# Kernel optimization log

Hardware: AMD Instinct MI355X
Metric: run time of the kernel (lower is better)

The kernel has to match this reference:

```python
import jax, jax.numpy as jnp
import numpy as np
from math import ceil

N = 20000   # nodes
E = 320000  # edges
D = 128     # num_features == num_hidden
K = ceil(N * 0.1)  # 2000 PMA seeds


def _gcn(x, W, b, src, dst):
    # PyG GCNConv: add self-loops, symmetric deg^-1/2 normalization, sum-aggregate, bias
    n = x.shape[0]
    sl = jnp.arange(n)
    s = jnp.concatenate([src, sl])
    d = jnp.concatenate([dst, sl])
    deg = jax.ops.segment_sum(jnp.ones((s.shape[0],), x.dtype), d, num_segments=n)
    dinv = jax.lax.rsqrt(jnp.maximum(deg, 1e-12))
    norm = dinv[s] * dinv[d]
    h = x @ W
    return jax.ops.segment_sum(h[s] * norm[:, None], d, num_segments=n) + b


def _ln(x, g, b):
    m = jnp.mean(x, -1, keepdims=True)
    v = jnp.var(x, -1, keepdims=True)
    return (x - m) * jax.lax.rsqrt(v + 1e-5) * g + b


def setup_inputs() -> dict:
    key = jax.random.key(0)
    ks = jax.random.split(key, 32)
    w = lambda i, shape: jax.random.normal(ks[i], shape, jnp.float32) * 0.05
    z = lambda shape: jnp.zeros(shape, jnp.float32)
    o = lambda shape: jnp.ones(shape, jnp.float32)
    return {
        "x": jax.random.normal(ks[0], (N, D), jnp.float32),
        "edge_index": jax.random.randint(ks[1], (2, E), 0, N),
        "batch": jnp.zeros((N,), jnp.int32),
        "W1": w(2, (D, D)), "b1": z((D,)),
        "W2": w(3, (D, D)), "b2": z((D,)),
        "S": w(4, (1, K, D)),
        "Wq": w(5, (D, D)), "bq": z((D,)),
        "Wk": w(6, (D, D)), "bk": z((D,)),
        "Wv": w(7, (D, D)), "bv": z((D,)),
        "Wo": w(8, (D, D)), "bo": z((D,)),
        "g0": o((D,)), "be0": z((D,)),
        "g1": o((D,)), "be1": z((D,)),
        "Wl": w(9, (D, D)), "bl": z((D,)),
        "W3": w(10, (D, D)), "b3": z((D,)),
        "W4": w(11, (D, D)), "b4": z((D,)),
        "W5": w(12, (D, D)), "b5": z((D,)),
    }


def reference(x, edge_index, batch, W1, b1, W2, b2, S, Wq, bq, Wk, bk, Wv, bv,
              Wo, bo, g0, be0, g1, be1, Wl, bl, W3, b3, W4, b4, W5, b5):
    src, dst = edge_index[0], edge_index[1]
    h = jax.nn.relu(_gcn(x, W1, b1, src, dst))
    h = jax.nn.relu(_gcn(h, W2, b2, src, dst))
    # B=1 dense batch: mask all-true -> additive attention mask is 0
    Q = S @ Wq + bq                        # [1,K,D]
    Kd = _gcn(h, Wk, bk, src, dst)[None]   # [1,N,D]  (mab_conv='GCN')
    Vd = _gcn(h, Wv, bv, src, dst)[None]   # [1,N,D]
    score = jnp.einsum('bkd,bnd->bkn', Q, Kd) / jnp.sqrt(jnp.float32(D))
    A = jax.nn.softmax(score, axis=1)      # cluster=True: softmax over seed dim
    out = Q + jnp.einsum('bkn,bnd->bkd', A, Vd)
    out = _ln(out, g0, be0)
    out = out + jax.nn.relu(out @ Wo + bo)
    out = _ln(out, g1, be1)
    xl = out @ Wl + bl                     # [1,K,D]
    x_out = jnp.einsum('bkn,bkd->bnd', A, xl)[0]  # attn^T @ x -> [N,D], mask all-true
    h = jax.nn.relu(_gcn(x_out, W3, b3, src, dst))
    h = jax.nn.relu(_gcn(h, W4, b4, src, dst))
    return _gcn(h, W5, b5, src, dst)       # [N,D]
```

## Files before the change

### kernel.cpp

```cpp
#include <hip/hip_runtime.h>

#define NN 20000
#define EE 320000
#define KK 2000
#define KP 2048
#define SCALE 0.08838834764831845f
#define ZSPLIT 16
#define ACHUNKS 625

typedef const float* cfp;
typedef __attribute__((ext_vector_type(8))) short sh8;
typedef __attribute__((ext_vector_type(4))) float f32x4;

static __device__ __forceinline__ float4 ld4(const float* p){ return *reinterpret_cast<const float4*>(p); }
static __device__ __forceinline__ void st4(float* p, float4 v){ *reinterpret_cast<float4*>(p) = v; }

static __device__ __forceinline__ unsigned short f2bf(float f){
    unsigned int u = __float_as_uint(f);
    u = (u + 0x7FFFu + ((u >> 16) & 1u)) >> 16;
    return (unsigned short)u;
}
static __device__ __forceinline__ float bf2f(unsigned short h){
    return __uint_as_float(((unsigned int)h) << 16);
}
static __device__ __forceinline__ sh8 lds8(const unsigned short* p){ return *reinterpret_cast<const sh8*>(p); }

__global__ __launch_bounds__(256) void k_count(const int* dst, int* deg){
    int i = blockIdx.x*256 + threadIdx.x;
    if (i < EE) atomicAdd(&deg[dst[i]], 1);
}

__global__ __launch_bounds__(256) void k_dinv(const int* deg, float* dinv){
    int n = blockIdx.x*256 + threadIdx.x;
    if (n < NN) dinv[n] = rsqrtf((float)deg[n] + 1.0f);
}

__global__ __launch_bounds__(1024) void k_scan(const int* cnt, int* rows){
    __shared__ int part[1024];
    int t = threadIdx.x;
    int base = t*20;
    int s = 0;
    for (int i = 0; i < 20; ++i){ int idx = base+i; if (idx < NN) s += cnt[idx]; }
    part[t] = s; __syncthreads();
    for (int off = 1; off < 1024; off <<= 1){
        int v = (t >= off) ? part[t-off] : 0;
        __syncthreads();
        part[t] += v;
        __syncthreads();
    }
    int run = part[t] - s;
    for (int i = 0; i < 20; ++i){
        int idx = base+i;
        if (idx < NN){ rows[idx] = run; run += cnt[idx]; }
    }
    if (t == 0) rows[NN] = EE;
}

__global__ __launch_bounds__(256) void k_fill(const int* src, const int* dst, const int* rows,
                                              int* cursor, int* col){
    int i = blockIdx.x*256 + threadIdx.x;
    if (i < EE){
        int d = dst[i];
        int pos = rows[d] + atomicAdd(&cursor[d], 1);
        col[pos] = src[i];
    }
}

__global__ __launch_bounds__(256) void conv_wT(cfp w0, cfp w1, cfp w2, cfp w3, cfp w4, cfp w5, cfp w6,
                                               unsigned short* wts){
    const float* in;
    switch (blockIdx.z){
        case 0: in = w0; break; case 1: in = w1; break; case 2: in = w2; break;
        case 3: in = w3; break; case 4: in = w4; break; case 5: in = w5; break;
        default: in = w6; break;
    }
    unsigned short* out = wts + (size_t)blockIdx.z*16384;
    __shared__ float t[64][65];
    int r0 = blockIdx.x*64, c0 = blockIdx.y*64;
    int tid = threadIdx.x;
    for (int i = tid; i < 64*16; i += 256){
        int r = i >> 4, c4 = (i & 15) * 4;
        float4 v = ld4(in + (size_t)(r0+r)*128 + c0 + c4);
        t[r][c4+0]=v.x; t[r][c4+1]=v.y; t[r][c4+2]=v.z; t[r][c4+3]=v.w;
    }
    __syncthreads();
    for (int i = tid; i < 64*16; i += 256){
        int c = i >> 4, r4 = (i & 15) * 4;
        ushort4 o;
        o.x = f2bf(t[r4+0][c]); o.y = f2bf(t[r4+1][c]);
        o.z = f2bf(t[r4+2][c]); o.w = f2bf(t[r4+3][c]);
        *reinterpret_cast<ushort4*>(out + (size_t)(c0+c)*128 + r0 + r4) = o;
    }
}

__global__ __launch_bounds__(512) void gemm128(const float* __restrict__ A, const float* __restrict__ Wm,
                                               float* __restrict__ C, int M,
                                               const float* bias, const float* resid, int relu){
    __shared__ __align__(16) float Ws[128*132];
    __shared__ float As[64*129];
    int tid = threadIdx.x;
    int r0 = blockIdx.x*64;
    for (int i = tid; i < 128*32; i += 512){
        int r = i >> 5, c4 = (i & 31) * 4;
        float4 v = ld4(Wm + r*128 + c4);
        st4(&Ws[r*132 + c4], v);
    }
    for (int i = tid; i < 64*32; i += 512){
        int r = i >> 5, c4 = (i & 31) * 4;
        float4 v = (r0 + r < M) ? ld4(A + (size_t)(r0+r)*128 + c4) : make_float4(0,0,0,0);
        As[r*129 + c4+0] = v.x; As[r*129 + c4+1] = v.y;
        As[r*129 + c4+2] = v.z; As[r*129 + c4+3] = v.w;
    }
    __syncthreads();
    int a = tid >> 5;
    int b = tid & 31;
    float acc[4][4] = {};
    #pragma unroll 4
    for (int d = 0; d < 128; ++d){
        float4 w = ld4(&Ws[d*132 + 4*b]);
        float wv[4] = {w.x, w.y, w.z, w.w};
        float av[4];
        #pragma unroll
        for (int i = 0; i < 4; ++i) av[i] = As[(4*a+i)*129 + d];
        #pragma unroll
        for (int i = 0; i < 4; ++i)
            #pragma unroll
            for (int j = 0; j < 4; ++j)
                acc[i][j] += av[i]*wv[j];
    }
    int cc = 4*b;
    #pragma unroll
    for (int i = 0; i < 4; ++i){
        int r = r0 + 4*a + i;
        if (r < M){
            float v[4];
            #pragma unroll
            for (int j = 0; j < 4; ++j) v[j] = acc[i][j];
            if (bias){
                #pragma unroll
                for (int j = 0; j < 4; ++j) v[j] += bias[cc+j];
            }
            if (relu){
                #pragma unroll
                for (int j = 0; j < 4; ++j) v[j] = fmaxf(v[j], 0.f);
            }
            if (resid){
                float4 rv = ld4(resid + (size_t)r*128 + cc);
                v[0]+=rv.x; v[1]+=rv.y; v[2]+=rv.z; v[3]+=rv.w;
            }
            st4(C + (size_t)r*128 + cc, make_float4(v[0],v[1],v[2],v[3]));
        }
    }
}

__global__ __launch_bounds__(256) void tgemm(const unsigned short* __restrict__ A, int M,
                                             const unsigned short* __restrict__ Wt,
                                             const float* __restrict__ rscale,
                                             unsigned short* __restrict__ C){
    int tid = threadIdx.x;
    int wave = tid >> 6, lane = tid & 63;
    int wm = wave >> 1, wn = wave & 1;
    int m_base = blockIdx.x*64 + wm*32;
    int n_base = blockIdx.y*64 + wn*32;
    int l15 = lane & 15;
    int roff = (lane >> 4) * 8;
    const unsigned short* ap0 = A + (size_t)(m_base + l15)*128 + roff;
    const unsigned short* ap1 = ap0 + 16*128;
    const unsigned short* b0p = Wt + (size_t)(n_base + l15)*128 + roff;
    const unsigned short* b1p = b0p + 16*128;
    f32x4 acc00 = (f32x4)0.f, acc01 = (f32x4)0.f, acc10 = (f32x4)0.f, acc11 = (f32x4)0.f;
    #pragma unroll
    for (int r = 0; r < 128; r += 32){
        sh8 a0 = lds8(ap0 + r);
        sh8 a1 = lds8(ap1 + r);
        sh8 b0 = lds8(b0p + r);
        sh8 b1 = lds8(b1p + r);
        acc00 = __builtin_amdgcn_mfma_f32_16x16x32_bf16(a0, b0, acc00, 0, 0, 0);
        acc01 = __builtin_amdgcn_mfma_f32_16x16x32_bf16(a0, b1, acc01, 0, 0, 0);
        acc10 = __builtin_amdgcn_mfma_f32_16x16x32_bf16(a1, b0, acc10, 0, 0, 0);
        acc11 = __builtin_amdgcn_mfma_f32_16x16x32_bf16(a1, b1, acc11, 0, 0, 0);
    }
    int rq = (lane >> 4) * 4;
    f32x4 accs[2][2] = {{acc00, acc01},{acc10, acc11}};
    #pragma unroll
    for (int mi = 0; mi < 2; ++mi){
        #pragma unroll
        for (int ni = 0; ni < 2; ++ni){
            f32x4 a = accs[mi][ni];
            int gn = n_base + ni*16 + l15;
            #pragma unroll
            for (int reg = 0; reg < 4; ++reg){
                int gm = m_base + mi*16 + rq + reg;
                if (gm < M) C[(size_t)gm*128 + gn] = f2bf(a[reg] * (rscale ? rscale[gm] : 1.f));
            }
        }
    }
}

__global__ __launch_bounds__(256) void gcn_agg_bf(const unsigned short* __restrict__ y, const float* __restrict__ dinv,
                                                  const int* __restrict__ rows, const int* __restrict__ col,
                                                  const float* __restrict__ bias, void* __restrict__ outv,
                                                  int relu, int out_fp32){
    int wid = (int)((blockIdx.x*256 + threadIdx.x) >> 6);
    int lane = threadIdx.x & 63;
    if (wid >= NN) return;
    int f = lane*2;
    ushort2 u = *reinterpret_cast<const ushort2*>(y + (size_t)wid*128 + f);
    float ax = bf2f(u.x), ay = bf2f(u.y);
    int s = rows[wid], e = rows[wid+1];
    int j = s;
    int e4 = s + ((e - s) & ~3);
    for (; j < e4; j += 4){
        int c0 = col[j], c1 = col[j+1], c2 = col[j+2], c3 = col[j+3];
        ushort2 v0 = *reinterpret_cast<const ushort2*>(y + (size_t)c0*128 + f);
        ushort2 v1 = *reinterpret_cast<const ushort2*>(y + (size_t)c1*128 + f);
        ushort2 v2 = *reinterpret_cast<const ushort2*>(y + (size_t)c2*128 + f);
        ushort2 v3 = *reinterpret_cast<const ushort2*>(y + (size_t)c3*128 + f);
        ax += bf2f(v0.x) + bf2f(v1.x) + bf2f(v2.x) + bf2f(v3.x);
        ay += bf2f(v0.y) + bf2f(v1.y) + bf2f(v2.y) + bf2f(v3.y);
    }
    for (; j < e; ++j){
        int c0 = col[j];
        ushort2 v0 = *reinterpret_cast<const ushort2*>(y + (size_t)c0*128 + f);
        ax += bf2f(v0.x); ay += bf2f(v0.y);
    }
    float dn = dinv[wid];
    float ox = ax*dn + bias[f];
    float oy = ay*dn + bias[f+1];
    if (relu){ ox = fmaxf(ox, 0.f); oy = fmaxf(oy, 0.f); }
    if (out_fp32){
        *reinterpret_cast<float2*>((float*)outv + (size_t)wid*128 + f) = make_float2(ox, oy);
    } else {
        ushort2 o; o.x = f2bf(ox); o.y = f2bf(oy);
        *reinterpret_cast<ushort2*>((unsigned short*)outv + (size_t)wid*128 + f) = o;
    }
}

__global__ __launch_bounds__(256) void conv_bf16(const float* __restrict__ in, unsigned short* __restrict__ out, int n4){
    int i = blockIdx.x*256 + threadIdx.x;
    if (i < n4){
        float4 v = ld4(in + (size_t)i*4);
        ushort4 o;
        o.x = f2bf(v.x); o.y = f2bf(v.y); o.z = f2bf(v.z); o.w = f2bf(v.w);
        *reinterpret_cast<ushort4*>(out + (size_t)i*4) = o;
    }
}

__global__ __launch_bounds__(256) void conv_bf16_T(const float* __restrict__ in, unsigned short* __restrict__ out,
                                                   int M, int ldout, const float* __restrict__ rscale){
    __shared__ float t[64][65];
    int r0 = blockIdx.x*64, c0 = blockIdx.y*64;
    int tid = threadIdx.x;
    for (int i = tid; i < 64*16; i += 256){
        int r = i >> 4, c4 = (i & 15) * 4;
        float4 v = (r0 + r < M) ? ld4(in + (size_t)(r0+r)*128 + c0 + c4) : make_float4(0,0,0,0);
        if (rscale && r0 + r < M){
            float sc = rscale[r0 + r];
            v.x *= sc; v.y *= sc; v.z *= sc; v.w *= sc;
        }
        t[r][c4+0]=v.x; t[r][c4+1]=v.y; t[r][c4+2]=v.z; t[r][c4+3]=v.w;
    }
    __syncthreads();
    for (int i = tid; i < 64*16; i += 256){
        int c = i >> 4, r4 = (i & 15) * 4;
        if (r0 + r4 < M){
            ushort4 o;
            o.x = f2bf(t[r4+0][c]); o.y = f2bf(t[r4+1][c]);
            o.z = f2bf(t[r4+2][c]); o.w = f2bf(t[r4+3][c]);
            *reinterpret_cast<ushort4*>(out + (size_t)(c0+c)*ldout + r0 + r4) = o;
        }
    }
}

__global__ __launch_bounds__(256) void k_rcp32(const float* __restrict__ zp, float* __restrict__ zinv){
    int n = blockIdx.x*256 + threadIdx.x;
    if (n < NN){
        float s = 0.f;
        #pragma unroll
        for (int y = 0; y < 32; ++y) s += zp[(size_t)y*NN + n];
        zinv[n] = 1.f / s;
    }
}

__global__ __launch_bounds__(256) void s_gemm_exp(const unsigned short* __restrict__ Kb,
                                                  const unsigned short* __restrict__ Qb2,
                                                  unsigned short* __restrict__ E, float* __restrict__ zpart){
    __shared__ unsigned short Es[64*68];
    int tid = threadIdx.x;
    int wave = tid >> 6, lane = tid & 63;
    int wm = wave >> 1, wn = wave & 1;
    int n_blk = blockIdx.x*64, k_blk = blockIdx.y*64;
    int l15 = lane & 15;
    int roff = (lane >> 4) * 8;
    const unsigned short* ap0 = Kb + (size_t)(n_blk + wm*32 + l15)*128 + roff;
    const unsigned short* ap1 = ap0 + 16*128;
    const unsigned short* bp0 = Qb2 + (size_t)(k_blk + wn*32 + l15)*128 + roff;
    const unsigned short* bp1 = bp0 + 16*128;
    f32x4 acc00 = (f32x4)0.f, acc01 = (f32x4)0.f, acc10 = (f32x4)0.f, acc11 = (f32x4)0.f;
    #pragma unroll
    for (int r = 0; r < 128; r += 32){
        sh8 a0 = lds8(ap0 + r);
        sh8 a1 = lds8(ap1 + r);
        sh8 b0 = lds8(bp0 + r);
        sh8 b1 = lds8(bp1 + r);
        acc00 = __builtin_amdgcn_mfma_f32_16x16x32_bf16(a0, b0, acc00, 0, 0, 0);
        acc01 = __builtin_amdgcn_mfma_f32_16x16x32_bf16(a0, b1, acc01, 0, 0, 0);
        acc10 = __builtin_amdgcn_mfma_f32_16x16x32_bf16(a1, b0, acc10, 0, 0, 0);
        acc11 = __builtin_amdgcn_mfma_f32_16x16x32_bf16(a1, b1, acc11, 0, 0, 0);
    }
    int rq = (lane >> 4) * 4;
    f32x4 accs[2][2] = {{acc00, acc01},{acc10, acc11}};
    #pragma unroll
    for (int mi = 0; mi < 2; ++mi){
        #pragma unroll
        for (int ni = 0; ni < 2; ++ni){
            f32x4 a = accs[mi][ni];
            int c_loc = wn*32 + ni*16 + l15;
            bool kv = (k_blk + c_loc) < KK;
            #pragma unroll
            for (int reg = 0; reg < 4; ++reg){
                int r_loc = wm*32 + mi*16 + rq + reg;
                float e = kv ? __expf(a[reg]*SCALE) : 0.f;
                Es[r_loc*68 + c_loc] = f2bf(e);
            }
        }
    }
    __syncthreads();
    if (tid < 64){
        int n = n_blk + tid;
        if (n < NN){
            float s = 0.f;
            #pragma unroll 8
            for (int j = 0; j < 64; ++j) s += bf2f(Es[tid*68 + j]);
            zpart[(size_t)blockIdx.y*NN + n] = s;
        }
    }
    for (int i = tid; i < 512; i += 256){
        int r = i >> 3, c8 = (i & 7) * 8;
        if (n_blk + r < NN){
            ushort4 lo = *reinterpret_cast<const ushort4*>(&Es[r*68 + c8]);
            ushort4 hi = *reinterpret_cast<const ushort4*>(&Es[r*68 + c8 + 4]);
            unsigned short* dst = E + (size_t)(n_blk + r)*KP + k_blk + c8;
            *reinterpret_cast<ushort4*>(dst) = lo;
            *reinterpret_cast<ushort4*>(dst + 4) = hi;
        }
    }
}

__global__ __launch_bounds__(256) void attn_gemm(const unsigned short* __restrict__ E,
                                                 const unsigned short* __restrict__ Vt,
                                                 float* __restrict__ part){
    __shared__ unsigned short As[64*36];
    int tid = threadIdx.x;
    int wave = tid >> 6, lane = tid & 63;
    int kk0 = blockIdx.x*64;
    int per = (ACHUNKS + ZSPLIT - 1) / ZSPLIT;
    int c0 = blockIdx.y*per;
    int c1 = min(ACHUNKS, c0 + per);
    int l15 = lane & 15;
    int q8 = (lane >> 4) * 8;
    int d0 = wave*32;
    int n_l = tid & 31;
    int k8 = (tid >> 5) * 8;
    f32x4 acc[4][2];
    #pragma unroll
    for (int g = 0; g < 4; ++g){ acc[g][0] = (f32x4)0.f; acc[g][1] = (f32x4)0.f; }
    const unsigned short* ebase = E + (size_t)n_l*KP + kk0 + k8;
    const unsigned short* vb0p = Vt + (size_t)(d0 + l15)*NN + q8;
    const unsigned short* vb1p = vb0p + (size_t)16*NN;
    sh8 etmp = lds8(ebase + (size_t)c0*32*KP);
    sh8 vb0 = lds8(vb0p + c0*32);
    sh8 vb1 = lds8(vb1p + c0*32);
    for (int ch = c0; ch < c1; ++ch){
        unsigned short tmp[8];
        *reinterpret_cast<sh8*>(tmp) = etmp;
        #pragma unroll
        for (int j = 0; j < 8; ++j) As[(k8 + j)*36 + n_l] = tmp[j];
        __syncthreads();
        sh8 etn = (sh8)0, vbn0 = (sh8)0, vbn1 = (sh8)0;
        if (ch + 1 < c1){
            etn  = lds8(ebase + (size_t)(ch+1)*32*KP);
            vbn0 = lds8(vb0p + (ch+1)*32);
            vbn1 = lds8(vb1p + (ch+1)*32);
        }
        #pragma unroll
        for (int g = 0; g < 4; ++g){
            const unsigned short* ap = &As[(g*16 + l15)*36 + q8];
            union { struct { ushort4 lo, hi; } u; sh8 v; } af;
            af.u.lo = *reinterpret_cast<const ushort4*>(ap);
            af.u.hi = *reinterpret_cast<const ushort4*>(ap + 4);
            acc[g][0] = __builtin_amdgcn_mfma_f32_16x16x32_bf16(af.v, vb0, acc[g][0], 0, 0, 0);
            acc[g][1] = __builtin_amdgcn_mfma_f32_16x16x32_bf16(af.v, vb1, acc[g][1], 0, 0, 0);
        }
        __syncthreads();
        etmp = etn; vb0 = vbn0; vb1 = vbn1;
    }
    float* pbase = part + (size_t)blockIdx.y*KK*128;
    int rq = (lane >> 4) * 4;
    #pragma unroll
    for (int g = 0; g < 4; ++g){
        #pragma unroll
        for (int ni = 0; ni < 2; ++ni){
            int d = d0 + ni*16 + l15;
            #pragma unroll
            for (int reg = 0; reg < 4; ++reg){
                int kk = kk0 + g*16 + rq + reg;
                if (kk < KK) pbase[(size_t)kk*128 + d] = acc[g][ni][reg];
            }
        }
    }
}

__global__ __launch_bounds__(256) void xout_gemm(const unsigned short* __restrict__ E,
                                                 const unsigned short* __restrict__ B,
                                                 const float* __restrict__ zinv,
                                                 unsigned short* __restrict__ xr){
    int tid = threadIdx.x;
    int wave = tid >> 6, lane = tid & 63;
    int wm = wave >> 1, wn = wave & 1;
    int m_base = blockIdx.x*64 + wm*32;
    int n_base = blockIdx.y*64 + wn*32;
    int l15 = lane & 15;
    int roff = (lane >> 4) * 8;
    const unsigned short* ap0 = E + (size_t)(m_base + l15)*KP + roff;
    const unsigned short* ap1 = ap0 + (size_t)16*KP;
    const unsigned short* bp0 = B + (size_t)(n_base + l15)*KP + roff;
    const unsigned short* bp1 = bp0 + (size_t)16*KP;
    f32x4 acc00 = (f32x4)0.f, acc01 = (f32x4)0.f, acc10 = (f32x4)0.f, acc11 = (f32x4)0.f;
    sh8 a0 = lds8(ap0),      a1 = lds8(ap1),      a2 = lds8(ap0 + 32), a3 = lds8(ap1 + 32);
    sh8 b0 = lds8(bp0),      b1 = lds8(bp1),      b2 = lds8(bp0 + 32), b3 = lds8(bp1 + 32);
    for (int r = 0; r < KP; r += 64){
        int rn = r + 64;
        sh8 na0 = (sh8)0, na1 = (sh8)0, na2 = (sh8)0, na3 = (sh8)0;
        sh8 nb0 = (sh8)0, nb1 = (sh8)0, nb2 = (sh8)0, nb3 = (sh8)0;
        if (rn < KP){
            na0 = lds8(ap0 + rn);      na1 = lds8(ap1 + rn);
            na2 = lds8(ap0 + rn + 32); na3 = lds8(ap1 + rn + 32);
            nb0 = lds8(bp0 + rn);      nb1 = lds8(bp1 + rn);
            nb2 = lds8(bp0 + rn + 32); nb3 = lds8(bp1 + rn + 32);
        }
        acc00 = __builtin_amdgcn_mfma_f32_16x16x32_bf16(a0, b0, acc00, 0, 0, 0);
        acc01 = __builtin_amdgcn_mfma_f32_16x16x32_bf16(a0, b1, acc01, 0, 0, 0);
        acc10 = __builtin_amdgcn_mfma_f32_16x16x32_bf16(a1, b0, acc10, 0, 0, 0);
        acc11 = __builtin_amdgcn_mfma_f32_16x16x32_bf16(a1, b1, acc11, 0, 0, 0);
        acc00 = __builtin_amdgcn_mfma_f32_16x16x32_bf16(a2, b2, acc00, 0, 0, 0);
        acc01 = __builtin_amdgcn_mfma_f32_16x16x32_bf16(a2, b3, acc01, 0, 0, 0);
        acc10 = __builtin_amdgcn_mfma_f32_16x16x32_bf16(a3, b2, acc10, 0, 0, 0);
        acc11 = __builtin_amdgcn_mfma_f32_16x16x32_bf16(a3, b3, acc11, 0, 0, 0);
        a0 = na0; a1 = na1; a2 = na2; a3 = na3;
        b0 = nb0; b1 = nb1; b2 = nb2; b3 = nb3;
    }
    int rq = (lane >> 4) * 4;
    f32x4 accs[2][2] = {{acc00, acc01},{acc10, acc11}};
    #pragma unroll
    for (int mi = 0; mi < 2; ++mi){
        #pragma unroll
        for (int ni = 0; ni < 2; ++ni){
            f32x4 a = accs[mi][ni];
            int gn = n_base + ni*16 + l15;
            #pragma unroll
            for (int reg = 0; reg < 4; ++reg){
                int gm = m_base + mi*16 + rq + reg;
                if (gm < NN) xr[(size_t)gm*128 + gn] = f2bf(a[reg]*zinv[gm]);
            }
        }
    }
}

__global__ __launch_bounds__(128) void ln_ker(const float* __restrict__ in, int nparts,
                                              const float* __restrict__ resid,
                                              const float* __restrict__ g, const float* __restrict__ be,
                                              float* __restrict__ out){
    __shared__ float rs[128], rq[128];
    int r = blockIdx.x, t = threadIdx.x;
    float v = 0.f;
    for (int p = 0; p < nparts; ++p) v += in[(size_t)p*KK*128 + r*128 + t];
    if (resid) v += resid[r*128 + t];
    rs[t] = v; rq[t] = v*v;
    __syncthreads();
    for (int off = 64; off > 0; off >>= 1){
        if (t < off){ rs[t] += rs[t+off]; rq[t] += rq[t+off]; }
        __syncthreads();
    }
    float mean = rs[0]*(1.f/128.f);
    float var = rq[0]*(1.f/128.f) - mean*mean;
    out[r*128 + t] = (v - mean)*rsqrtf(var + 1e-5f)*g[t] + be[t];
}

extern "C" void kernel_launch(void* const* d_in, const int* in_sizes, int n_in,
                              void* d_out, int out_size, void* d_ws, size_t ws_size,
                              hipStream_t stream){
    cfp x  = (cfp)d_in[0];
    const int* ei = (const int*)d_in[1];
    const int* esrc = ei;
    const int* edst = ei + EE;
    cfp W1=(cfp)d_in[3], b1=(cfp)d_in[4], W2=(cfp)d_in[5], b2=(cfp)d_in[6];
    cfp S =(cfp)d_in[7];
    cfp Wq=(cfp)d_in[8],  bq=(cfp)d_in[9],  Wk=(cfp)d_in[10], bk=(cfp)d_in[11];
    cfp Wv=(cfp)d_in[12], bv=(cfp)d_in[13], Wo=(cfp)d_in[14], bo=(cfp)d_in[15];
    cfp g0=(cfp)d_in[16], be0=(cfp)d_in[17], g1=(cfp)d_in[18], be1=(cfp)d_in[19];
    cfp Wl=(cfp)d_in[20], bl=(cfp)d_in[21], W3=(cfp)d_in[22], b3=(cfp)d_in[23];
    cfp W4=(cfp)d_in[24], b4=(cfp)d_in[25], W5=(cfp)d_in[26], b5=(cfp)d_in[27];

    char* wsb = (char*)d_ws;
    const size_t MB = 1048576;
    int*   deg    = (int*)  (wsb + 0);
    float* dinv   = (float*)(wsb + 81920);
    int*   rows   = (int*)  (wsb + 163840);
    int*   cursor = (int*)  (wsb + 245760);
    int*   col    = (int*)  (wsb + 327680);
    float* Qb     = (float*)(wsb + 2*MB);
    float* o1     = (float*)(wsb + 3*MB);
    float* o2     = (float*)(wsb + 4*MB);
    float* o3     = (float*)(wsb + 5*MB);
    float* xlb    = (float*)(wsb + 6*MB);
    float* zpart  = (float*)(wsb + 7*MB);
    float* zinv   = (float*)(wsb + 10*MB);
    unsigned short* Wts = (unsigned short*)(wsb + 10*MB + 131072);
    unsigned short* Qbf = (unsigned short*)(wsb + 11*MB);
    unsigned short* xlt = (unsigned short*)(wsb + 11*MB + 524288);
    unsigned short* xbf = (unsigned short*)(wsb + 12*MB);
    unsigned short* h1  = (unsigned short*)(wsb + 17*MB);
    unsigned short* h2  = (unsigned short*)(wsb + 22*MB);
    unsigned short* ybuf= (unsigned short*)(wsb + 27*MB);
    unsigned short* Kbf = (unsigned short*)(wsb + 32*MB);
    unsigned short* Vtz = (unsigned short*)(wsb + 37*MB);
    float* NB3    = (float*)(wsb + 42*MB);
    float* part   = (float*)(wsb + 52*MB);
    unsigned short* E = (unsigned short*)(wsb + 68*MB);
    float* outp   = (float*)d_out;
    unsigned short* h3 = xbf;
    unsigned short* h4 = h1;
    unsigned short* xr = Kbf;

    (void)hipMemsetAsync(deg, 0, NN*sizeof(int), stream);
    (void)hipMemsetAsync(cursor, 0, NN*sizeof(int), stream);

    k_count<<<1250, 256, 0, stream>>>(edst, deg);
    k_dinv<<<79, 256, 0, stream>>>(deg, dinv);
    k_scan<<<1, 1024, 0, stream>>>(deg, rows);
    k_fill<<<1250, 256, 0, stream>>>(esrc, edst, rows, cursor, col);

    conv_wT<<<dim3(2,2,7), 256, 0, stream>>>(W1, W2, Wk, Wv, W3, W4, W5, Wts);
    conv_bf16<<<2500, 256, 0, stream>>>(x, xbf, NN*32);
    unsigned short* W1t = Wts;
    unsigned short* W2t = Wts + 16384;
    unsigned short* Wkt = Wts + 2*16384;
    unsigned short* Wvt = Wts + 3*16384;
    unsigned short* W3t = Wts + 4*16384;
    unsigned short* W4t = Wts + 5*16384;
    unsigned short* W5t = Wts + 6*16384;

    const int GN = 313;
    const int GK = 32;

    tgemm<<<dim3(GN,2), 256, 0, stream>>>(xbf, NN, W1t, dinv, ybuf);
    gcn_agg_bf<<<5000, 256, 0, stream>>>(ybuf, dinv, rows, col, b1, h1, 1, 0);
    tgemm<<<dim3(GN,2), 256, 0, stream>>>(h1, NN, W2t, dinv, ybuf);
    gcn_agg_bf<<<5000, 256, 0, stream>>>(ybuf, dinv, rows, col, b2, h2, 1, 0);
    tgemm<<<dim3(GN,2), 256, 0, stream>>>(h2, NN, Wkt, dinv, ybuf);
    gcn_agg_bf<<<5000, 256, 0, stream>>>(ybuf, dinv, rows, col, bk, Kbf, 0, 0);
    gemm128<<<GK, 512, 0, stream>>>(S, Wq, Qb, KK, bq, nullptr, 0);
    conv_bf16<<<250, 256, 0, stream>>>(Qb, Qbf, KK*32);
    s_gemm_exp<<<dim3(GN, GK), 256, 0, stream>>>(Kbf, Qbf, E, zpart);
    k_rcp32<<<79, 256, 0, stream>>>(zpart, zinv);
    tgemm<<<dim3(GN,2), 256, 0, stream>>>(h2, NN, Wvt, dinv, ybuf);
    gcn_agg_bf<<<5000, 256, 0, stream>>>(ybuf, dinv, rows, col, bv, NB3, 0, 1);
    conv_bf16_T<<<dim3(GN, 2), 256, 0, stream>>>(NB3, Vtz, NN, NN, zinv);
    attn_gemm<<<dim3(GK, ZSPLIT), 256, 0, stream>>>(E, Vtz, part);
    ln_ker<<<KK, 128, 0, stream>>>(part, ZSPLIT, Qb, g0, be0, o1);
    gemm128<<<GK, 512, 0, stream>>>(o1, Wo, o2, KK, bo, o1, 1);
    ln_ker<<<KK, 128, 0, stream>>>(o2, 1, nullptr, g1, be1, o3);
    gemm128<<<GK, 512, 0, stream>>>(o3, Wl, xlb, KK, bl, nullptr, 0);
    conv_bf16_T<<<dim3(GK, 2), 256, 0, stream>>>(xlb, xlt, KK, KP, nullptr);
    xout_gemm<<<dim3(GN, 2), 256, 0, stream>>>(E, xlt, zinv, xr);
    tgemm<<<dim3(GN,2), 256, 0, stream>>>(xr, NN, W3t, dinv, ybuf);
    gcn_agg_bf<<<5000, 256, 0, stream>>>(ybuf, dinv, rows, col, b3, h3, 1, 0);
    tgemm<<<dim3(GN,2), 256, 0, stream>>>(h3, NN, W4t, dinv, ybuf);
    gcn_agg_bf<<<5000, 256, 0, stream>>>(ybuf, dinv, rows, col, b4, h4, 1, 0);
    tgemm<<<dim3(GN,2), 256, 0, stream>>>(h4, NN, W5t, dinv, ybuf);
    gcn_agg_bf<<<5000, 256, 0, stream>>>(ybuf, dinv, rows, col, b5, outp, 0, 1);
}
```

Measured before the change: 638.2 us.

## Fold W3 into seed features, split-K xout GEMM, and unroll aggregation by eight

```diff
diff --git a/kernel.cpp b/kernel.cpp
--- a/kernel.cpp
+++ b/kernel.cpp
@@ -209,15 +209,16 @@
     float ax = bf2f(u.x), ay = bf2f(u.y);
     int s = rows[wid], e = rows[wid+1];
     int j = s;
-    int e4 = s + ((e - s) & ~3);
-    for (; j < e4; j += 4){
-        int c0 = col[j], c1 = col[j+1], c2 = col[j+2], c3 = col[j+3];
-        ushort2 v0 = *reinterpret_cast<const ushort2*>(y + (size_t)c0*128 + f);
-        ushort2 v1 = *reinterpret_cast<const ushort2*>(y + (size_t)c1*128 + f);
-        ushort2 v2 = *reinterpret_cast<const ushort2*>(y + (size_t)c2*128 + f);
-        ushort2 v3 = *reinterpret_cast<const ushort2*>(y + (size_t)c3*128 + f);
-        ax += bf2f(v0.x) + bf2f(v1.x) + bf2f(v2.x) + bf2f(v3.x);
-        ay += bf2f(v0.y) + bf2f(v1.y) + bf2f(v2.y) + bf2f(v3.y);
+    int e8 = s + ((e - s) & ~7);
+    for (; j < e8; j += 8){
+        ushort2 v[8];
+        #pragma unroll
+        for (int q = 0; q < 8; ++q){
+            int c = col[j+q];
+            v[q] = *reinterpret_cast<const ushort2*>(y + (size_t)c*128 + f);
+        }
+        #pragma unroll
+        for (int q = 0; q < 8; ++q){ ax += bf2f(v[q].x); ay += bf2f(v[q].y); }
     }
     for (; j < e; ++j){
         int c0 = col[j];
@@ -272,13 +273,16 @@
     }
 }
 
-__global__ __launch_bounds__(256) void k_rcp32(const float* __restrict__ zp, float* __restrict__ zinv){
+__global__ __launch_bounds__(256) void k_rcp32(const float* __restrict__ zp, const float* __restrict__ dinv,
+                                               float* __restrict__ zinv, float* __restrict__ zdinv){
     int n = blockIdx.x*256 + threadIdx.x;
     if (n < NN){
         float s = 0.f;
         #pragma unroll
         for (int y = 0; y < 32; ++y) s += zp[(size_t)y*NN + n];
-        zinv[n] = 1.f / s;
+        float zi = 1.f / s;
+        zinv[n] = zi;
+        zdinv[n] = zi * dinv[n];
     }
 }
 
@@ -413,27 +417,27 @@
 
 __global__ __launch_bounds__(256) void xout_gemm(const unsigned short* __restrict__ E,
                                                  const unsigned short* __restrict__ B,
-                                                 const float* __restrict__ zinv,
-                                                 unsigned short* __restrict__ xr){
+                                                 float* __restrict__ xpart){
     int tid = threadIdx.x;
     int wave = tid >> 6, lane = tid & 63;
     int wm = wave >> 1, wn = wave & 1;
     int m_base = blockIdx.x*64 + wm*32;
     int n_base = blockIdx.y*64 + wn*32;
+    int kz = blockIdx.z*1024;
     int l15 = lane & 15;
     int roff = (lane >> 4) * 8;
-    const unsigned short* ap0 = E + (size_t)(m_base + l15)*KP + roff;
+    const unsigned short* ap0 = E + (size_t)(m_base + l15)*KP + kz + roff;
     const unsigned short* ap1 = ap0 + (size_t)16*KP;
-    const unsigned short* bp0 = B + (size_t)(n_base + l15)*KP + roff;
+    const unsigned short* bp0 = B + (size_t)(n_base + l15)*KP + kz + roff;
     const unsigned short* bp1 = bp0 + (size_t)16*KP;
     f32x4 acc00 = (f32x4)0.f, acc01 = (f32x4)0.f, acc10 = (f32x4)0.f, acc11 = (f32x4)0.f;
     sh8 a0 = lds8(ap0),      a1 = lds8(ap1),      a2 = lds8(ap0 + 32), a3 = lds8(ap1 + 32);
     sh8 b0 = lds8(bp0),      b1 = lds8(bp1),      b2 = lds8(bp0 + 32), b3 = lds8(bp1 + 32);
-    for (int r = 0; r < KP; r += 64){
+    for (int r = 0; r < 1024; r += 64){
         int rn = r + 64;
         sh8 na0 = (sh8)0, na1 = (sh8)0, na2 = (sh8)0, na3 = (sh8)0;
         sh8 nb0 = (sh8)0, nb1 = (sh8)0, nb2 = (sh8)0, nb3 = (sh8)0;
-        if (rn < KP){
+        if (rn < 1024){
             na0 = lds8(ap0 + rn);      na1 = lds8(ap1 + rn);
             na2 = lds8(ap0 + rn + 32); na3 = lds8(ap1 + rn + 32);
             nb0 = lds8(bp0 + rn);      nb1 = lds8(bp1 + rn);
@@ -450,6 +454,7 @@
         a0 = na0; a1 = na1; a2 = na2; a3 = na3;
         b0 = nb0; b1 = nb1; b2 = nb2; b3 = nb3;
     }
+    float* pbase = xpart + (size_t)blockIdx.z*NN*128;
     int rq = (lane >> 4) * 4;
     f32x4 accs[2][2] = {{acc00, acc01},{acc10, acc11}};
     #pragma unroll
@@ -461,9 +466,26 @@
             #pragma unroll
             for (int reg = 0; reg < 4; ++reg){
                 int gm = m_base + mi*16 + rq + reg;
-                if (gm < NN) xr[(size_t)gm*128 + gn] = f2bf(a[reg]*zinv[gm]);
+                if (gm < NN) pbase[(size_t)gm*128 + gn] = a[reg];
             }
         }
+    }
+}
+
+__global__ __launch_bounds__(256) void xred(const float* __restrict__ xp, const float* __restrict__ zdinv,
+                                            unsigned short* __restrict__ out){
+    int i = blockIdx.x*256 + threadIdx.x;
+    if (i < NN*32){
+        int row = i >> 5;
+        float4 p0 = ld4(xp + (size_t)i*4);
+        float4 p1 = ld4(xp + (size_t)NN*128 + (size_t)i*4);
+        float sc = zdinv[row];
+        ushort4 o;
+        o.x = f2bf((p0.x + p1.x)*sc);
+        o.y = f2bf((p0.y + p1.y)*sc);
+        o.z = f2bf((p0.z + p1.z)*sc);
+        o.w = f2bf((p0.w + p1.w)*sc);
+        *reinterpret_cast<ushort4*>(out + (size_t)i*4) = o;
     }
 }
 
@@ -516,9 +538,10 @@
     float* xlb    = (float*)(wsb + 6*MB);
     float* zpart  = (float*)(wsb + 7*MB);
     float* zinv   = (float*)(wsb + 10*MB);
-    unsigned short* Wts = (unsigned short*)(wsb + 10*MB + 131072);
-    unsigned short* Qbf = (unsigned short*)(wsb + 11*MB);
-    unsigned short* xlt = (unsigned short*)(wsb + 11*MB + 524288);
+    float* zdinv  = (float*)(wsb + 10*MB + 131072);
+    unsigned short* Wts  = (unsigned short*)(wsb + 10*MB + 262144);
+    unsigned short* Qbf  = (unsigned short*)(wsb + 11*MB);
+    unsigned short* xlt3 = (unsigned short*)(wsb + 11*MB + 524288);
     unsigned short* xbf = (unsigned short*)(wsb + 12*MB);
     unsigned short* h1  = (unsigned short*)(wsb + 17*MB);
     unsigned short* h2  = (unsigned short*)(wsb + 22*MB);
@@ -526,15 +549,16 @@
     unsigned short* Kbf = (unsigned short*)(wsb + 32*MB);
     unsigned short* Vtz = (unsigned short*)(wsb + 37*MB);
     float* NB3    = (float*)(wsb + 42*MB);
-    float* part   = (float*)(wsb + 52*MB);
-    unsigned short* E = (unsigned short*)(wsb + 68*MB);
+    float* part   = (float*)(wsb + 42*MB);
+    float* xpart  = (float*)(wsb + 42*MB);
+    unsigned short* E = (unsigned short*)(wsb + 62*MB);
     float* outp   = (float*)d_out;
     unsigned short* h3 = xbf;
     unsigned short* h4 = h1;
-    unsigned short* xr = Kbf;
 
     (void)hipMemsetAsync(deg, 0, NN*sizeof(int), stream);
     (void)hipMemsetAsync(cursor, 0, NN*sizeof(int), stream);
+    (void)hipMemsetAsync(xlt3, 0, 128*KP*sizeof(unsigned short), stream);
 
     k_count<<<1250, 256, 0, stream>>>(edst, deg);
     k_dinv<<<79, 256, 0, stream>>>(deg, dinv);
@@ -547,7 +571,6 @@
     unsigned short* W2t = Wts + 16384;
     unsigned short* Wkt = Wts + 2*16384;
     unsigned short* Wvt = Wts + 3*16384;
-    unsigned short* W3t = Wts + 4*16384;
     unsigned short* W4t = Wts + 5*16384;
     unsigned short* W5t = Wts + 6*16384;
 
@@ -563,7 +586,7 @@
     gemm128<<<GK, 512, 0, stream>>>(S, Wq, Qb, KK, bq, nullptr, 0);
     conv_bf16<<<250, 256, 0, stream>>>(Qb, Qbf, KK*32);
     s_gemm_exp<<<dim3(GN, GK), 256, 0, stream>>>(Kbf, Qbf, E, zpart);
-    k_rcp32<<<79, 256, 0, stream>>>(zpart, zinv);
+    k_rcp32<<<79, 256, 0, stream>>>(zpart, dinv, zinv, zdinv);
     tgemm<<<dim3(GN,2), 256, 0, stream>>>(h2, NN, Wvt, dinv, ybuf);
     gcn_agg_bf<<<5000, 256, 0, stream>>>(ybuf, dinv, rows, col, bv, NB3, 0, 1);
     conv_bf16_T<<<dim3(GN, 2), 256, 0, stream>>>(NB3, Vtz, NN, NN, zinv);
@@ -572,9 +595,10 @@
     gemm128<<<GK, 512, 0, stream>>>(o1, Wo, o2, KK, bo, o1, 1);
     ln_ker<<<KK, 128, 0, stream>>>(o2, 1, nullptr, g1, be1, o3);
     gemm128<<<GK, 512, 0, stream>>>(o3, Wl, xlb, KK, bl, nullptr, 0);
-    conv_bf16_T<<<dim3(GK, 2), 256, 0, stream>>>(xlb, xlt, KK, KP, nullptr);
-    xout_gemm<<<dim3(GN, 2), 256, 0, stream>>>(E, xlt, zinv, xr);
-    tgemm<<<dim3(GN,2), 256, 0, stream>>>(xr, NN, W3t, dinv, ybuf);
+    gemm128<<<GK, 512, 0, stream>>>(xlb, W3, o1, KK, nullptr, nullptr, 0);
+    conv_bf16_T<<<dim3(GK, 2), 256, 0, stream>>>(o1, xlt3, KK, KP, nullptr);
+    xout_gemm<<<dim3(GN, 2, 2), 256, 0, stream>>>(E, xlt3, xpart);
+    xred<<<2500, 256, 0, stream>>>(xpart, zdinv, ybuf);
     gcn_agg_bf<<<5000, 256, 0, stream>>>(ybuf, dinv, rows, col, b3, h3, 1, 0);
     tgemm<<<dim3(GN,2), 256, 0, stream>>>(h3, NN, W4t, dinv, ybuf);
     gcn_agg_bf<<<5000, 256, 0, stream>>>(ybuf, dinv, rows, col, b4, h4, 1, 0);
```

Result: no change. 632.7 us (-0.9%).
